# Kernel tuning notes

Hardware: AMD Instinct MI355X
Metric: run time of the kernel (lower is better)

The kernel has to match this reference:

```python
import jax, jax.numpy as jnp
import numpy as np

B, C, D, L, H, K, S, OUT = 8, 2048, 128, 3, 4, 200, 64, 24
d = D // H  # d_head = 32


def _ln(x, g, b):
    m = x.mean(-1, keepdims=True)
    v = ((x - m) ** 2).mean(-1, keepdims=True)
    return (x - m) / jnp.sqrt(v + 1e-5) * g + b


def _gelu(x):
    return jax.nn.gelu(x, approximate=False)  # torch default exact GELU


def setup_inputs() -> dict:
    key = jax.random.key(0)
    ks = iter(jax.random.split(key, 32))
    def nrm(shape, std=0.02):
        return jax.random.normal(next(ks), shape, jnp.float32) * std
    return {
        "x": jax.random.uniform(next(ks), (B, C), jnp.float32) * 5.0,
        "role_emb": nrm((C, D)),
        "filler_w": nrm((D,), 0.1),
        "qW": nrm((L, D, D), 0.05), "qb": jnp.zeros((L, D)),
        "kW": nrm((L, D, D), 0.05), "kb": jnp.zeros((L, D)),
        "vW": nrm((L, D, D), 0.05), "vb": jnp.zeros((L, D)),
        "oW": nrm((L, D, D), 0.05), "ob": jnp.zeros((L, D)),
        "relW1": nrm((L, 3 * d, d), 0.05), "relb1": jnp.zeros((L, d)),
        "relW2": nrm((L, d), 0.05), "relb2": jnp.zeros((L,)),
        "ln1_g": jnp.ones((L, D)), "ln1_b": jnp.zeros((L, D)),
        "ln2_g": jnp.ones((L, D)), "ln2_b": jnp.zeros((L, D)),
        "ffnW1": nrm((L, D, 4 * D), 0.05), "ffnb1": jnp.zeros((L, 4 * D)),
        "ffnW2": nrm((L, 4 * D, D), 0.05), "ffnb2": jnp.zeros((L, D)),
        "slots": nrm((S, D)),
        "memln_g": jnp.ones((D,)), "memln_b": jnp.zeros((D,)),
        "task_q": nrm((D,)),
        "headW": nrm((D, OUT), 0.05), "headb": jnp.zeros((OUT,)),
        "top_k": K,
    }


def _forward(x, role_emb, filler_w, qW, qb, kW, kb, vW, vb, oW, ob,
             relW1, relb1, relW2, relb2, ln1_g, ln1_b, ln2_g, ln2_b,
             ffnW1, ffnb1, ffnW2, ffnb2, slots, memln_g, memln_b,
             task_q, headW, headb, top_k):
    Bx = x.shape[0]
    x_log = jnp.log1p(jnp.maximum(x, 0.0))
    vals, idx = jax.lax.top_k(x_log, top_k)            # [B,K] top intensities
    roles = role_emb[idx]                              # [B,K,D]
    fillers = _gelu(vals[..., None] * filler_w)        # Linear(1,D,bias=False)+GELU
    b = roles * fillers                                # hadamard binding [B,K,D]
    sc_d = jnp.float32(d) ** 0.5
    for l in range(qW.shape[0]):
        q = (b @ qW[l] + qb[l]).reshape(Bx, -1, H, d).transpose(0, 2, 1, 3)
        k = (b @ kW[l] + kb[l]).reshape(Bx, -1, H, d).transpose(0, 2, 1, 3)
        v = (b @ vW[l] + vb[l]).reshape(Bx, -1, H, d).transpose(0, 2, 1, 3)
        # MLP_rel([q_i || k_j || q_i*k_j]) decomposed over the 3d input blocks
        W1q, W1k, W1i = relW1[l][:d], relW1[l][d:2 * d], relW1[l][2 * d:]
        qt = jnp.einsum('bhie,ef->bhif', q, W1q)       # [B,H,K,d]
        kt = jnp.einsum('bhje,ef->bhjf', k, W1k)       # [B,H,K,d]
        itm = jnp.einsum('bhie,bhje,ef->bhijf', q, k, W1i)  # pairwise [B,H,K,K,d]
        hrel = _gelu(qt[:, :, :, None, :] + kt[:, :, None, :, :] + itm + relb1[l])
        scores = (jnp.einsum('bhijf,f->bhij', hrel, relW2[l]) + relb2[l]) / sc_d
        attn = jax.nn.softmax(scores, axis=-1)
        o = jnp.einsum('bhij,bhjd->bhid', attn, v)
        o = o.transpose(0, 2, 1, 3).reshape(Bx, -1, D) @ oW[l] + ob[l]
        b = _ln(b + o, ln1_g[l], ln1_b[l])
        f = _gelu(b @ ffnW1[l] + ffnb1[l]) @ ffnW2[l] + ffnb2[l]
        b = _ln(b + f, ln2_g[l], ln2_b[l])
    sc_D = jnp.float32(D) ** 0.5
    ra = jax.nn.softmax(jnp.einsum('bcd,d->bc', b, task_q) / sc_D, axis=-1)
    h = jnp.einsum('bc,bcd->bd', ra, b)                # task-query readout
    ma = jax.nn.softmax(jnp.einsum('sd,bcd->bsc', slots, b) / sc_D, axis=-1)
    mem = _ln(jnp.einsum('bsc,bcd->bsd', ma, b).mean(axis=1), memln_g, memln_b)
    return (h + mem) @ headW + headb                   # [B,OUT]


def reference(x, role_emb, filler_w, qW, qb, kW, kb, vW, vb, oW, ob,
              relW1, relb1, relW2, relb2, ln1_g, ln1_b, ln2_g, ln2_b,
              ffnW1, ffnb1, ffnW2, ffnb2, slots, memln_g, memln_b,
              task_q, headW, headb, top_k):
    return _forward(x, role_emb, filler_w, qW, qb, kW, kb, vW, vb, oW, ob,
                    relW1, relb1, relW2, relb2, ln1_g, ln1_b, ln2_g, ln2_b,
                    ffnW1, ffnb1, ffnW2, ffnb2, slots, memln_g, memln_b,
                    task_q, headW, headb, top_k)
```

## Files before the change

kernel.cpp:

```cpp
#include <hip/hip_runtime.h>
#include <math.h>

#define BQ 8
#define CC 2048
#define DDIM 128
#define LLAY 3
#define HH 4
#define KK 200
#define SSLOT 64
#define OUTN 24
#define DH 32

typedef __bf16 bf16_t;
typedef __bf16 bf16x8 __attribute__((ext_vector_type(8)));
typedef float f32x4 __attribute__((ext_vector_type(4)));

__device__ __forceinline__ float fastrcp(float x) {
#if __has_builtin(__builtin_amdgcn_rcpf)
  return __builtin_amdgcn_rcpf(x);
#else
  return 1.0f / x;
#endif
}
__device__ __forceinline__ float fastexp2(float x) {
#if __has_builtin(__builtin_amdgcn_exp2f)
  return __builtin_amdgcn_exp2f(x);
#else
  return exp2f(x);
#endif
}
__device__ __forceinline__ float fgelu2(float x) {
  float s = x * x;
  float inner = fmaf(0.044715f * s, x, x);
  float e = fastexp2(inner * 2.302118610509359f);
  float r = fastrcp(1.f + e);
  return fmaf(-x, r, x);
}
__device__ __forceinline__ float egelu(float x) {
  return 0.5f * x * (1.f + erff(x * 0.7071067811865476f));
}

__global__ __launch_bounds__(256) void prep_kernel(
    const float* __restrict__ qW, const float* __restrict__ kW,
    const float* __restrict__ vW, const float* __restrict__ oW,
    const float* __restrict__ fW1, const float* __restrict__ fW2,
    bf16_t* __restrict__ wtb,
    const float* __restrict__ x, const float* __restrict__ role_emb,
    const float* __restrict__ fw, float* __restrict__ btok,
    bf16_t* __restrict__ btokbf) {
  __shared__ float Ts[64][65];
  __shared__ float svals[KK];
  __shared__ int sidx[KK];
  __shared__ int red[4];
  __shared__ int cnt;
  const int blk = blockIdx.x, tid = threadIdx.x;
  if (blk < 144) {
    const int t = blk;
    const float* src; bf16_t* dst; int N, K, k0, n0;
    if (t < 48) {
      int which = t / 12, rem = t % 12;
      int l = rem >> 2, tt = rem & 3;
      N = 128; K = 128; k0 = (tt >> 1) * 64; n0 = (tt & 1) * 64;
      src = (which == 0 ? qW : which == 1 ? kW : which == 2 ? vW : oW) + l * 16384;
      dst = wtb + which * 49152 + l * 16384;
    } else if (t < 96) {
      int t2 = t - 48, l = t2 >> 4, tt = t2 & 15;
      N = 512; K = 128; k0 = (tt >> 3) * 64; n0 = (tt & 7) * 64;
      src = fW1 + l * 65536;
      dst = wtb + 196608 + l * 65536;
    } else {
      int t3 = t - 96, l = t3 >> 4, tt = t3 & 15;
      N = 128; K = 512; k0 = (tt >> 1) * 64; n0 = (tt & 1) * 64;
      src = fW2 + l * 65536;
      dst = wtb + 393216 + l * 65536;
    }
#pragma unroll
    for (int i = 0; i < 16; ++i) {
      int u = tid + i * 256;
      int r = u >> 6, c = u & 63;
      Ts[r][c] = src[(size_t)(k0 + r) * N + n0 + c];
    }
    __syncthreads();
#pragma unroll
    for (int i = 0; i < 16; ++i) {
      int u = tid + i * 256;
      int rn = u >> 6, ck = u & 63;
      dst[(size_t)(n0 + rn) * K + k0 + ck] = (bf16_t)Ts[ck][rn];
    }
    return;
  }
  const int b = blk - 144;
  float xv[8]; unsigned xb[8];
#pragma unroll
  for (int t = 0; t < 8; t++) {
    float v = x[b * CC + t * 256 + tid];
    xv[t] = v;
    xb[t] = __float_as_uint(v);
  }
  unsigned lo = 0u, hi = 0x7f800000u;
  while (lo < hi) {
    unsigned mid = (lo + hi) >> 1;
    int c = 0;
#pragma unroll
    for (int t = 0; t < 8; t++) c += (xb[t] > mid) ? 1 : 0;
#pragma unroll
    for (int m = 1; m <= 32; m <<= 1) c += __shfl_xor(c, m);
    if ((tid & 63) == 0) red[tid >> 6] = c;
    __syncthreads();
    int ct = red[0] + red[1] + red[2] + red[3];
    __syncthreads();
    if (ct >= KK) lo = mid + 1; else hi = mid;
  }
  const unsigned thr = lo;
  if (tid == 0) cnt = 0;
  __syncthreads();
#pragma unroll
  for (int t = 0; t < 8; t++) {
    if (xb[t] > thr) {
      int p = atomicAdd(&cnt, 1);
      svals[p] = log1pf(xv[t]);
      sidx[p] = t * 256 + tid;
    }
  }
  __syncthreads();
#pragma unroll
  for (int t = 0; t < 8; t++) {
    if (xb[t] == thr) {
      int p = atomicAdd(&cnt, 1);
      if (p < KK) {
        svals[p] = log1pf(xv[t]);
        sidx[p] = t * 256 + tid;
      }
    }
  }
  __syncthreads();
  for (int u = tid; u < KK * DDIM; u += 256) {
    int dd = u & 127, t = u >> 7;
    float v = svals[t];
    float fill = egelu(v * fw[dd]);
    float val = role_emb[(size_t)sidx[t] * DDIM + dd] * fill;
    btok[(size_t)b * KK * DDIM + u] = val;
    btokbf[(size_t)b * KK * DDIM + u] = (bf16_t)val;
  }
}

__global__ __launch_bounds__(256) void qkv_mfma(const bf16_t* __restrict__ A,
    const bf16_t* __restrict__ qWt, const float* __restrict__ qb,
    const bf16_t* __restrict__ kWt, const float* __restrict__ kb,
    const bf16_t* __restrict__ vWt, const float* __restrict__ vb,
    bf16_t* __restrict__ qo, bf16_t* __restrict__ ko, bf16_t* __restrict__ vo) {
  __shared__ __align__(16) bf16_t Alds[32 * 16 * 8];
  __shared__ __align__(16) bf16_t Blds[128 * 16 * 8];
  const int tid = threadIdx.x, m0 = blockIdx.x * 32, z = blockIdx.y;
  const bf16_t* Wt; const float* bias; bf16_t* C;
  if (z == 0) { Wt = qWt; bias = qb; C = qo; }
  else if (z == 1) { Wt = kWt; bias = kb; C = ko; }
  else { Wt = vWt; bias = vb; C = vo; }
#pragma unroll
  for (int it = 0; it < 2; ++it) {
    int u = tid + it * 256;
    int row = u >> 4, kc = u & 15;
    uint4 d = *(const uint4*)(A + (size_t)(m0 + row) * 128 + kc * 8);
    *(uint4*)&Alds[(row * 16 + (kc ^ (row & 7))) * 8] = d;
  }
#pragma unroll
  for (int it = 0; it < 8; ++it) {
    int u = tid + it * 256;
    int col = u >> 4, kcb = u & 15;
    uint4 d = *(const uint4*)(Wt + (size_t)col * 128 + kcb * 8);
    *(uint4*)&Blds[(col * 16 + (kcb ^ (col & 7))) * 8] = d;
  }
  __syncthreads();
  const int w = tid >> 6, lane = tid & 63, fcol = lane & 15, g = lane >> 4;
  const int wr = w & 1, wn = w >> 1;
  f32x4 acc[4];
#pragma unroll
  for (int ni = 0; ni < 4; ++ni) acc[ni] = (f32x4){0.f, 0.f, 0.f, 0.f};
#pragma unroll
  for (int ks = 0; ks < 4; ++ks) {
    const int arow = 16 * wr + fcol;
    bf16x8 a = *(const bf16x8*)&Alds[(arow * 16 + ((ks * 4 + g) ^ (arow & 7))) * 8];
#pragma unroll
    for (int ni = 0; ni < 4; ++ni) {
      const int bcol = wn * 64 + ni * 16 + fcol;
      bf16x8 b = *(const bf16x8*)&Blds[(bcol * 16 + ((ks * 4 + g) ^ (bcol & 7))) * 8];
      acc[ni] = __builtin_amdgcn_mfma_f32_16x16x32_bf16(a, b, acc[ni], 0, 0, 0);
    }
  }
#pragma unroll
  for (int ni = 0; ni < 4; ++ni) {
    const int col = wn * 64 + ni * 16 + fcol;
    const float bv = bias[col];
#pragma unroll
    for (int r = 0; r < 4; ++r) {
      const int row = m0 + 16 * wr + 4 * g + r;
      C[(size_t)row * 128 + col] = (bf16_t)(acc[ni][r] + bv);
    }
  }
}

__global__ __launch_bounds__(256, 3) void rel_attn_mfma(
    const bf16_t* __restrict__ qbf, const bf16_t* __restrict__ kbf,
    const bf16_t* __restrict__ vbf,
    const float* __restrict__ W1g, const float* __restrict__ b1g,
    const float* __restrict__ w2p, bf16_t* __restrict__ o) {
  __shared__ __align__(16) bf16_t ksh[208 * 32];
  __shared__ __align__(16) bf16_t vtsh[32 * 224];
  __shared__ __align__(16) bf16_t psh[8 * 224];
  __shared__ __align__(16) bf16_t W1ki[32 * 66];
  __shared__ __align__(16) bf16_t qsh[8 * 32];
  __shared__ __align__(16) bf16_t qtshb[8 * 32];
  const int tid = threadIdx.x;
  const int bh = blockIdx.y, bb = bh >> 2, h = bh & 3;
  const int i0 = blockIdx.x * 8;
  const bf16_t* kgb = kbf + (size_t)(bb * KK) * DDIM + h * DH;
  const bf16_t* vgb = vbf + (size_t)(bb * KK) * DDIM + h * DH;
  const bf16_t* qgb = qbf + (size_t)(bb * KK) * DDIM + h * DH;
#pragma unroll
  for (int it = 0; it < 4; ++it) {
    int u = tid + it * 256;
    if (u < 832) {
      int j = u >> 2, bi = u & 3;
      uint4 d = {0u, 0u, 0u, 0u};
      if (j < KK) d = *(const uint4*)(kgb + (size_t)j * DDIM + bi * 8);
      *(uint4*)&ksh[j * 32 + (bi ^ ((j >> 1) & 3)) * 8] = d;
    }
  }
#pragma unroll
  for (int it = 0; it < 13; ++it) {
    int u = tid + it * 256;
    int jp = u >> 5, f = u & 31;
    int j0 = jp * 2;
    bf16_t a0 = (j0 < KK) ? vgb[(size_t)j0 * DDIM + f] : (bf16_t)0.f;
    bf16_t a1 = (j0 + 1 < KK) ? vgb[(size_t)(j0 + 1) * DDIM + f] : (bf16_t)0.f;
    union { bf16_t h2[2]; unsigned uu; } pk;
    pk.h2[0] = a0; pk.h2[1] = a1;
    *(unsigned*)&vtsh[f * 224 + j0] = pk.uu;
  }
  {
    int f = tid >> 3, cp = tid & 7;
    *(unsigned*)&vtsh[f * 224 + 208 + cp * 2] = 0u;
  }
  if (tid < 64) {
    int r = tid >> 3, cp = tid & 7;
    *(unsigned*)&psh[r * 224 + 208 + cp * 2] = 0u;
  }
#pragma unroll
  for (int it = 0; it < 8; ++it) {
    int u = tid + it * 256;
    int sel = u & 1, f = (u >> 1) & 31, e = u >> 6;
    W1ki[e * 66 + f * 2 + sel] = (bf16_t)W1g[(32 + sel * 32 + e) * 32 + f];
  }
  if (tid < 128) {
    int il = tid >> 4, ep = tid & 15;
    *(unsigned*)&qsh[il * 32 + ep * 2] =
        *(const unsigned*)(qgb + (size_t)(i0 + il) * DDIM + ep * 2);
  }
  __syncthreads();
  {
    int il = tid >> 5, f = tid & 31;
    float a = b1g[f];
#pragma unroll
    for (int e = 0; e < 32; ++e)
      a = fmaf((float)qsh[il * 32 + e], W1g[e * 32 + f], a);
    qtshb[il * 32 + f] = (bf16_t)a;
  }
  __syncthreads();
  const int w = tid >> 6, lane = tid & 63;
  const int fcol = lane & 15, g = lane >> 4;
  const float w2c = 0.17677669529663687f * 1.4426950408889634f;
  float4 w2a = *(const float4*)(w2p + 4 * g);
  float4 w2b = *(const float4*)(w2p + 16 + 4 * g);
  w2a.x *= w2c; w2a.y *= w2c; w2a.z *= w2c; w2a.w *= w2c;
  w2b.x *= w2c; w2b.y *= w2c; w2b.z *= w2c; w2b.w *= w2c;
#pragma unroll 1
  for (int c = 0; c < 2; ++c) {
    const int il = w * 2 + c;
    bf16x8 qv8 = *(const bf16x8*)&qsh[il * 32 + g * 8];
    bf16x8 bw0, bw1;
#pragma unroll
    for (int e8 = 0; e8 < 8; ++e8) {
      int e = g * 8 + e8;
      float qe = (float)qv8[e8];
      union { unsigned u; bf16_t h[2]; } k0_, k1_;
      k0_.u = *(const unsigned*)&W1ki[e * 66 + fcol * 2];
      k1_.u = *(const unsigned*)&W1ki[e * 66 + (fcol + 16) * 2];
      bw0[e8] = (bf16_t)fmaf(qe, (float)k0_.h[1], (float)k0_.h[0]);
      bw1[e8] = (bf16_t)fmaf(qe, (float)k1_.h[1], (float)k1_.h[0]);
    }
    const bf16_t* qtp = &qtshb[il * 32];
    const f32x4 cin0 = {(float)qtp[4 * g + 0], (float)qtp[4 * g + 1],
                        (float)qtp[4 * g + 2], (float)qtp[4 * g + 3]};
    const f32x4 cin1 = {(float)qtp[16 + 4 * g + 0], (float)qtp[16 + 4 * g + 1],
                        (float)qtp[16 + 4 * g + 2], (float)qtp[16 + 4 * g + 3]};
    float s[13];
#pragma unroll
    for (int jt = 0; jt < 13; ++jt) {
      int j = jt * 16 + fcol;
      bf16x8 af = *(const bf16x8*)&ksh[j * 32 + (g ^ ((j >> 1) & 3)) * 8];
      f32x4 acc0 = __builtin_amdgcn_mfma_f32_16x16x32_bf16(bw0, af, cin0, 0, 0, 0);
      f32x4 acc1 = __builtin_amdgcn_mfma_f32_16x16x32_bf16(bw1, af, cin1, 0, 0, 0);
      float t0 = fgelu2(acc0[0]) * w2a.x;
      t0 = fmaf(fgelu2(acc0[1]), w2a.y, t0);
      float t1 = fgelu2(acc0[2]) * w2a.z;
      t1 = fmaf(fgelu2(acc0[3]), w2a.w, t1);
      float t2 = fgelu2(acc1[0]) * w2b.x;
      t2 = fmaf(fgelu2(acc1[1]), w2b.y, t2);
      float t3 = fgelu2(acc1[2]) * w2b.z;
      t3 = fmaf(fgelu2(acc1[3]), w2b.w, t3);
      float t = (t0 + t1) + (t2 + t3);
      t += __shfl_xor(t, 16);
      t += __shfl_xor(t, 32);
      s[jt] = t;
    }
    if (fcol >= 8) s[12] = -1e30f;
    float m = s[0];
#pragma unroll
    for (int jt = 1; jt < 13; ++jt) m = fmaxf(m, s[jt]);
    m = fmaxf(m, __shfl_xor(m, 1));
    m = fmaxf(m, __shfl_xor(m, 2));
    m = fmaxf(m, __shfl_xor(m, 4));
    m = fmaxf(m, __shfl_xor(m, 8));
    float l = 0.f;
#pragma unroll
    for (int jt = 0; jt < 13; ++jt) {
      float p = fastexp2(s[jt] - m);
      s[jt] = p;
      l += p;
    }
    l += __shfl_xor(l, 1);
    l += __shfl_xor(l, 2);
    l += __shfl_xor(l, 4);
    l += __shfl_xor(l, 8);
    const float inv = fastrcp(l);
    if (g == 0) {
#pragma unroll
      for (int jt = 0; jt < 13; ++jt)
        psh[il * 224 + jt * 16 + fcol] = (bf16_t)(s[jt] * inv);
    }
  }
  __syncthreads();
  if (w < 2) {
    f32x4 acc = {0.f, 0.f, 0.f, 0.f};
#pragma unroll
    for (int ks = 0; ks < 7; ++ks) {
      bf16x8 ap;
      if (fcol < 8) ap = *(const bf16x8*)&psh[fcol * 224 + ks * 32 + g * 8];
      else { bf16x8 z = {}; ap = z; }
      bf16x8 bv = *(const bf16x8*)&vtsh[(w * 16 + fcol) * 224 + ks * 32 + g * 8];
      acc = __builtin_amdgcn_mfma_f32_16x16x32_bf16(ap, bv, acc, 0, 0, 0);
    }
    if (g < 2) {
#pragma unroll
      for (int r = 0; r < 4; ++r) {
        int i = i0 + g * 4 + r;
        o[(size_t)(bb * KK + i) * DDIM + h * DH + w * 16 + fcol] = (bf16_t)acc[r];
      }
    }
  }
}

__global__ __launch_bounds__(512) void tail_fused(const bf16_t* __restrict__ obufbf,
    const bf16_t* __restrict__ oWt, const float* __restrict__ ob,
    const float* __restrict__ ln1g, const float* __restrict__ ln1b,
    const bf16_t* __restrict__ W1t, const float* __restrict__ b1,
    const bf16_t* __restrict__ W2t, const float* __restrict__ b2,
    const float* __restrict__ ln2g, const float* __restrict__ ln2b,
    float* __restrict__ btok, bf16_t* __restrict__ btokbf,
    const bf16_t* __restrict__ nqWt, const float* __restrict__ nqb,
    const bf16_t* __restrict__ nkWt, const float* __restrict__ nkb,
    const bf16_t* __restrict__ nvWt, const float* __restrict__ nvb,
    bf16_t* __restrict__ nqo, bf16_t* __restrict__ nko, bf16_t* __restrict__ nvo) {
  __shared__ __align__(16) bf16_t Alds[64 * 16 * 8];
  __shared__ __align__(16) bf16_t Blds[128 * 16 * 8];
  __shared__ __align__(16) bf16_t Hlds[64 * 512];
  __shared__ float lnredS[64][2], lnredQ[64][2];
  const int tid = threadIdx.x, m0 = blockIdx.x * 64;
  const int w = tid >> 6, lane = tid & 63, fcol = lane & 15, g = lane >> 4;
  const int wrow = w & 3, whalf = w >> 2;
#pragma unroll
  for (int it = 0; it < 2; ++it) {
    int u = tid + it * 512;
    int row = u >> 4, kc = u & 15;
    uint4 d = *(const uint4*)(obufbf + (size_t)(m0 + row) * 128 + kc * 8);
    *(uint4*)&Alds[(row * 16 + (kc ^ (row & 7))) * 8] = d;
  }
#pragma unroll
  for (int it = 0; it < 4; ++it) {
    int u = tid + it * 512;
    int col = u >> 4, kcb = u & 15;
    uint4 d = *(const uint4*)(oWt + (size_t)col * 128 + kcb * 8);
    *(uint4*)&Blds[(col * 16 + (kcb ^ (col & 7))) * 8] = d;
  }
  __syncthreads();
  f32x4 acc[4];
#pragma unroll
  for (int ni = 0; ni < 4; ++ni) acc[ni] = (f32x4){0.f, 0.f, 0.f, 0.f};
  const int arow = 16 * wrow + fcol;
#pragma unroll
  for (int ks = 0; ks < 4; ++ks) {
    bf16x8 a = *(const bf16x8*)&Alds[(arow * 16 + ((ks * 4 + g) ^ (arow & 7))) * 8];
#pragma unroll
    for (int ni = 0; ni < 4; ++ni) {
      const int bcol = whalf * 64 + ni * 16 + fcol;
      bf16x8 b = *(const bf16x8*)&Blds[(bcol * 16 + ((ks * 4 + g) ^ (bcol & 7))) * 8];
      acc[ni] = __builtin_amdgcn_mfma_f32_16x16x32_bf16(a, b, acc[ni], 0, 0, 0);
    }
  }
  float lnr[4][4];
  {
    float s_[4] = {0.f, 0.f, 0.f, 0.f}, q_[4] = {0.f, 0.f, 0.f, 0.f};
#pragma unroll
    for (int ni = 0; ni < 4; ++ni) {
      const int col = whalf * 64 + ni * 16 + fcol;
      const float bv = ob[col];
#pragma unroll
      for (int r = 0; r < 4; ++r) {
        const int row = m0 + 16 * wrow + 4 * g + r;
        float val = acc[ni][r] + bv + btok[(size_t)row * 128 + col];
        lnr[ni][r] = val;
        s_[r] += val; q_[r] += val * val;
      }
    }
#pragma unroll
    for (int m = 1; m <= 8; m <<= 1)
#pragma unroll
      for (int r = 0; r < 4; ++r) {
        s_[r] += __shfl_xor(s_[r], m); q_[r] += __shfl_xor(q_[r], m);
      }
    if (fcol == 0) {
#pragma unroll
      for (int r = 0; r < 4; ++r) {
        lnredS[16 * wrow + 4 * g + r][whalf] = s_[r];
        lnredQ[16 * wrow + 4 * g + r][whalf] = q_[r];
      }
    }
    __syncthreads();
    float mean[4], rs[4];
#pragma unroll
    for (int r = 0; r < 4; ++r) {
      const int rl = 16 * wrow + 4 * g + r;
      float S = lnredS[rl][0] + lnredS[rl][1];
      float Q = lnredQ[rl][0] + lnredQ[rl][1];
      mean[r] = S * (1.f / 128.f);
      rs[r] = rsqrtf(Q * (1.f / 128.f) - mean[r] * mean[r] + 1e-5f);
    }
#pragma unroll
    for (int ni = 0; ni < 4; ++ni) {
      const int col = whalf * 64 + ni * 16 + fcol;
      const float gv = ln1g[col], bv2 = ln1b[col];
#pragma unroll
      for (int r = 0; r < 4; ++r) {
        float v2 = (lnr[ni][r] - mean[r]) * rs[r] * gv + bv2;
        lnr[ni][r] = v2;
        const int rowL = 16 * wrow + 4 * g + r;
        Alds[(rowL * 16 + ((col >> 3) ^ (rowL & 7))) * 8 + (col & 7)] = (bf16_t)v2;
      }
    }
  }
  __syncthreads();
  for (int nc = 0; nc < 4; ++nc) {
#pragma unroll
    for (int it = 0; it < 4; ++it) {
      int u = tid + it * 512;
      int col = u >> 4, kcb = u & 15;
      uint4 d = *(const uint4*)(W1t + (size_t)(nc * 128 + col) * 128 + kcb * 8);
      *(uint4*)&Blds[(col * 16 + (kcb ^ (col & 7))) * 8] = d;
    }
    __syncthreads();
    f32x4 a1[4];
#pragma unroll
    for (int ni = 0; ni < 4; ++ni) a1[ni] = (f32x4){0.f, 0.f, 0.f, 0.f};
#pragma unroll
    for (int ks = 0; ks < 4; ++ks) {
      bf16x8 a = *(const bf16x8*)&Alds[(arow * 16 + ((ks * 4 + g) ^ (arow & 7))) * 8];
#pragma unroll
      for (int ni = 0; ni < 4; ++ni) {
        const int bcol = whalf * 64 + ni * 16 + fcol;
        bf16x8 b = *(const bf16x8*)&Blds[(bcol * 16 + ((ks * 4 + g) ^ (bcol & 7))) * 8];
        a1[ni] = __builtin_amdgcn_mfma_f32_16x16x32_bf16(a, b, a1[ni], 0, 0, 0);
      }
    }
#pragma unroll
    for (int ni = 0; ni < 4; ++ni) {
      const int c = nc * 128 + whalf * 64 + ni * 16 + fcol;
      const float bv = b1[c];
      const int kb = c >> 3, within = c & 7;
#pragma unroll
      for (int r = 0; r < 4; ++r) {
        const int row = 16 * wrow + 4 * g + r;
        const int kbs = kb ^ (row & 7);
        Hlds[row * 512 + kbs * 8 + within] = (bf16_t)egelu(a1[ni][r] + bv);
      }
    }
    __syncthreads();
  }
  f32x4 acc2[4];
#pragma unroll
  for (int ni = 0; ni < 4; ++ni) acc2[ni] = (f32x4){0.f, 0.f, 0.f, 0.f};
  for (int kc = 0; kc < 4; ++kc) {
#pragma unroll
    for (int it = 0; it < 4; ++it) {
      int u = tid + it * 512;
      int col = u >> 4, kcb = u & 15;
      uint4 d = *(const uint4*)(W2t + (size_t)col * 512 + kc * 128 + kcb * 8);
      *(uint4*)&Blds[(col * 16 + (kcb ^ (col & 7))) * 8] = d;
    }
    __syncthreads();
#pragma unroll
    for (int ks = 0; ks < 4; ++ks) {
      const int kb = kc * 16 + ks * 4 + g;
      const int kbs = kb ^ (arow & 7);
      bf16x8 a = *(const bf16x8*)&Hlds[arow * 512 + kbs * 8];
#pragma unroll
      for (int ni = 0; ni < 4; ++ni) {
        const int bcol = whalf * 64 + ni * 16 + fcol;
        bf16x8 b = *(const bf16x8*)&Blds[(bcol * 16 + ((ks * 4 + g) ^ (bcol & 7))) * 8];
        acc2[ni] = __builtin_amdgcn_mfma_f32_16x16x32_bf16(a, b, acc2[ni], 0, 0, 0);
      }
    }
    __syncthreads();
  }
  {
    float s_[4] = {0.f, 0.f, 0.f, 0.f}, q_[4] = {0.f, 0.f, 0.f, 0.f};
#pragma unroll
    for (int ni = 0; ni < 4; ++ni) {
      const int col = whalf * 64 + ni * 16 + fcol;
      const float bv = b2[col];
#pragma unroll
      for (int r = 0; r < 4; ++r) {
        float val = acc2[ni][r] + bv + lnr[ni][r];
        lnr[ni][r] = val;
        s_[r] += val; q_[r] += val * val;
      }
    }
#pragma unroll
    for (int m = 1; m <= 8; m <<= 1)
#pragma unroll
      for (int r = 0; r < 4; ++r) {
        s_[r] += __shfl_xor(s_[r], m); q_[r] += __shfl_xor(q_[r], m);
      }
    if (fcol == 0) {
#pragma unroll
      for (int r = 0; r < 4; ++r) {
        lnredS[16 * wrow + 4 * g + r][whalf] = s_[r];
        lnredQ[16 * wrow + 4 * g + r][whalf] = q_[r];
      }
    }
    __syncthreads();
    float mean[4], rs[4];
#pragma unroll
    for (int r = 0; r < 4; ++r) {
      const int rl = 16 * wrow + 4 * g + r;
      float S = lnredS[rl][0] + lnredS[rl][1];
      float Q = lnredQ[rl][0] + lnredQ[rl][1];
      mean[r] = S * (1.f / 128.f);
      rs[r] = rsqrtf(Q * (1.f / 128.f) - mean[r] * mean[r] + 1e-5f);
    }
#pragma unroll
    for (int ni = 0; ni < 4; ++ni) {
      const int col = whalf * 64 + ni * 16 + fcol;
      const float gv = ln2g[col], bv2 = ln2b[col];
#pragma unroll
      for (int r = 0; r < 4; ++r) {
        const int row = m0 + 16 * wrow + 4 * g + r;
        float oval = (lnr[ni][r] - mean[r]) * rs[r] * gv + bv2;
        btok[(size_t)row * 128 + col] = oval;
        btokbf[(size_t)row * 128 + col] = (bf16_t)oval;
        if (nqWt) {
          const int rowL = 16 * wrow + 4 * g + r;
          Alds[(rowL * 16 + ((col >> 3) ^ (rowL & 7))) * 8 + (col & 7)] = (bf16_t)oval;
        }
      }
    }
  }
  if (nqWt) {
    __syncthreads();
    const bf16_t* Ws[3] = {nqWt, nkWt, nvWt};
    const float* bs[3] = {nqb, nkb, nvb};
    bf16_t* Cs[3] = {nqo, nko, nvo};
    for (int zz = 0; zz < 3; ++zz) {
      const bf16_t* Wt = Ws[zz];
#pragma unroll
      for (int it = 0; it < 4; ++it) {
        int u = tid + it * 512;
        int col = u >> 4, kcb = u & 15;
        uint4 d = *(const uint4*)(Wt + (size_t)col * 128 + kcb * 8);
        *(uint4*)&Blds[(col * 16 + (kcb ^ (col & 7))) * 8] = d;
      }
      __syncthreads();
      f32x4 aq[4];
#pragma unroll
      for (int ni = 0; ni < 4; ++ni) aq[ni] = (f32x4){0.f, 0.f, 0.f, 0.f};
#pragma unroll
      for (int ks = 0; ks < 4; ++ks) {
        bf16x8 a = *(const bf16x8*)&Alds[(arow * 16 + ((ks * 4 + g) ^ (arow & 7))) * 8];
#pragma unroll
        for (int ni = 0; ni < 4; ++ni) {
          const int bcol = whalf * 64 + ni * 16 + fcol;
          bf16x8 b = *(const bf16x8*)&Blds[(bcol * 16 + ((ks * 4 + g) ^ (bcol & 7))) * 8];
          aq[ni] = __builtin_amdgcn_mfma_f32_16x16x32_bf16(a, b, aq[ni], 0, 0, 0);
        }
      }
      const float* bias = bs[zz];
      bf16_t* C = Cs[zz];
#pragma unroll
      for (int ni = 0; ni < 4; ++ni) {
        const int col = whalf * 64 + ni * 16 + fcol;
        const float bv = bias[col];
#pragma unroll
        for (int r = 0; r < 4; ++r) {
          const int row = m0 + 16 * wrow + 4 * g + r;
          C[(size_t)row * 128 + col] = (bf16_t)(aq[ni][r] + bv);
        }
      }
      __syncthreads();
    }
  }
}

__global__ __launch_bounds__(256) void readout_fused(const float* __restrict__ B,
    const bf16_t* __restrict__ Bbf, const float* __restrict__ slots,
    const float* __restrict__ task_q, const float* __restrict__ memg,
    const float* __restrict__ membt, const float* __restrict__ headW,
    const float* __restrict__ headb, float* __restrict__ out) {
  __shared__ __align__(16) bf16_t Ssh[64 * 16 * 8];
  __shared__ __align__(16) bf16_t Bsh[208 * 128];
  __shared__ float wcsh[4][208];
  __shared__ __align__(16) float tq[128];
  __shared__ float ras[KK];
  __shared__ float wc[208];
  __shared__ float red1[4], red2[4];
  __shared__ float hv2[256], mv2[256];
  __shared__ float hv[128], mv[128], rv[128];
  __shared__ float stats[2];
  const int b = blockIdx.x, tid = threadIdx.x;
  const int w = tid >> 6, lane = tid & 63, fcol = lane & 15, g = lane >> 4;
#pragma unroll
  for (int it = 0; it < 4; ++it) {
    int u = tid + it * 256;
    int row = u >> 4, kb = u & 15;
    const float* sp = slots + (size_t)row * 128 + kb * 8;
    bf16_t tmp[8];
#pragma unroll
    for (int e = 0; e < 8; ++e) tmp[e] = (bf16_t)sp[e];
    *(uint4*)&Ssh[(row * 16 + (kb ^ (row & 7))) * 8] = *(uint4*)tmp;
  }
#pragma unroll
  for (int it = 0; it < 13; ++it) {
    int u = tid + it * 256;
    int c = u >> 4, kb = u & 15;
    uint4 d = {0u, 0u, 0u, 0u};
    if (c < KK) d = *(const uint4*)(Bbf + (size_t)(b * KK + c) * 128 + kb * 8);
    *(uint4*)&Bsh[(c * 16 + (kb ^ (c & 7))) * 8] = d;
  }
  if (tid < 128) tq[tid] = task_q[tid];
  __syncthreads();
  {
    bf16x8 afr[4];
#pragma unroll
    for (int ks = 0; ks < 4; ++ks) {
      const int arow = 16 * w + fcol;
      afr[ks] = *(const bf16x8*)&Ssh[(arow * 16 + ((ks * 4 + g) ^ (arow & 7))) * 8];
    }
    f32x4 acc[13];
#pragma unroll
    for (int ct = 0; ct < 13; ++ct) {
      acc[ct] = (f32x4){0.f, 0.f, 0.f, 0.f};
#pragma unroll
      for (int ks = 0; ks < 4; ++ks) {
        const int bcol = ct * 16 + fcol;
        bf16x8 bb = *(const bf16x8*)&Bsh[(bcol * 16 + ((ks * 4 + g) ^ (bcol & 7))) * 8];
        acc[ct] = __builtin_amdgcn_mfma_f32_16x16x32_bf16(afr[ks], bb, acc[ct], 0, 0, 0);
      }
    }
    if (fcol >= 8) { acc[12][0] = -1e30f; acc[12][1] = -1e30f; acc[12][2] = -1e30f; acc[12][3] = -1e30f; }
    const float s2 = 0.08838834764831845f * 1.4426950408889634f;
    float wcp[13];
#pragma unroll
    for (int ct = 0; ct < 13; ++ct) wcp[ct] = 0.f;
#pragma unroll
    for (int r = 0; r < 4; ++r) {
      float m = acc[0][r];
#pragma unroll
      for (int ct = 1; ct < 13; ++ct) m = fmaxf(m, acc[ct][r]);
      m = fmaxf(m, __shfl_xor(m, 1));
      m = fmaxf(m, __shfl_xor(m, 2));
      m = fmaxf(m, __shfl_xor(m, 4));
      m = fmaxf(m, __shfl_xor(m, 8));
      float l = 0.f;
      float p[13];
#pragma unroll
      for (int ct = 0; ct < 13; ++ct) {
        p[ct] = fastexp2((acc[ct][r] - m) * s2);
        l += p[ct];
      }
      l += __shfl_xor(l, 1);
      l += __shfl_xor(l, 2);
      l += __shfl_xor(l, 4);
      l += __shfl_xor(l, 8);
      const float inv = fastrcp(l);
#pragma unroll
      for (int ct = 0; ct < 13; ++ct) wcp[ct] = fmaf(p[ct], inv, wcp[ct]);
    }
#pragma unroll
    for (int ct = 0; ct < 13; ++ct) {
      wcp[ct] += __shfl_xor(wcp[ct], 16);
      wcp[ct] += __shfl_xor(wcp[ct], 32);
      if (g == 0) wcsh[w][ct * 16 + fcol] = wcp[ct];
    }
  }
  float sc = -1e30f;
  if (tid < KK) {
    const float* br = B + (size_t)(b * KK + tid) * DDIM;
    float a = 0.f;
#pragma unroll
    for (int d4 = 0; d4 < 32; d4++) {
      float4 bb = *(const float4*)(br + d4 * 4);
      float4 ss = *(const float4*)(tq + d4 * 4);
      a += bb.x * ss.x + bb.y * ss.y + bb.z * ss.z + bb.w * ss.w;
    }
    sc = a * 0.08838834764831845f;
  }
  float mx = sc;
#pragma unroll
  for (int m = 1; m <= 32; m <<= 1) mx = fmaxf(mx, __shfl_xor(mx, m));
  if ((tid & 63) == 0) red1[tid >> 6] = mx;
  __syncthreads();
  mx = fmaxf(fmaxf(red1[0], red1[1]), fmaxf(red1[2], red1[3]));
  float p = (tid < KK) ? __expf(sc - mx) : 0.f;
  float sm = p;
#pragma unroll
  for (int m = 1; m <= 32; m <<= 1) sm += __shfl_xor(sm, m);
  if ((tid & 63) == 0) red2[tid >> 6] = sm;
  __syncthreads();
  sm = red2[0] + red2[1] + red2[2] + red2[3];
  if (tid < KK) ras[tid] = p / sm;
  if (tid < 208)
    wc[tid] = (wcsh[0][tid] + wcsh[1][tid] + wcsh[2][tid] + wcsh[3][tid]) * (1.f / 64.f);
  __syncthreads();
  {
    const int d = tid & 127, half = tid >> 7;
    float hd = 0.f, md = 0.f;
    const float* Bb = B + ((size_t)b * KK + half * 100) * DDIM + d;
    const float* rp = ras + half * 100;
    const float* wp = wc + half * 100;
#pragma unroll 2
    for (int c = 0; c < 100; ++c) {
      float bv = Bb[(size_t)c * DDIM];
      hd = fmaf(rp[c], bv, hd);
      md = fmaf(wp[c], bv, md);
    }
    hv2[tid] = hd; mv2[tid] = md;
  }
  __syncthreads();
  if (tid < 128) {
    hv[tid] = hv2[tid] + hv2[tid + 128];
    mv[tid] = mv2[tid] + mv2[tid + 128];
  }
  __syncthreads();
  if (tid < 64) {
    float x0 = mv[tid], x1 = mv[tid + 64];
    float s = x0 + x1, qq = x0 * x0 + x1 * x1;
#pragma unroll
    for (int m = 1; m <= 32; m <<= 1) { s += __shfl_xor(s, m); qq += __shfl_xor(qq, m); }
    if (tid == 0) { stats[0] = s; stats[1] = qq; }
  }
  __syncthreads();
  float mean = stats[0] * (1.f / 128.f);
  float var = stats[1] * (1.f / 128.f) - mean * mean;
  float rs = rsqrtf(var + 1e-5f);
  if (tid < 128) rv[tid] = hv[tid] + (mv[tid] - mean) * rs * memg[tid] + membt[tid];
  __syncthreads();
  if (tid < OUTN) {
    float a = headb[tid];
    for (int dd = 0; dd < 128; dd++) a = fmaf(rv[dd], headW[dd * OUTN + tid], a);
    out[b * OUTN + tid] = a;
  }
}

extern "C" void kernel_launch(void* const* d_in, const int* in_sizes, int n_in,
                              void* d_out, int out_size, void* d_ws, size_t ws_size,
                              hipStream_t stream) {
  (void)in_sizes; (void)n_in; (void)out_size; (void)ws_size;
  const float* x        = (const float*)d_in[0];
  const float* role_emb = (const float*)d_in[1];
  const float* filler_w = (const float*)d_in[2];
  const float* qW = (const float*)d_in[3];
  const float* qb = (const float*)d_in[4];
  const float* kW = (const float*)d_in[5];
  const float* kb = (const float*)d_in[6];
  const float* vW = (const float*)d_in[7];
  const float* vb = (const float*)d_in[8];
  const float* oW = (const float*)d_in[9];
  const float* ob = (const float*)d_in[10];
  const float* relW1 = (const float*)d_in[11];
  const float* relb1 = (const float*)d_in[12];
  const float* relW2 = (const float*)d_in[13];
  const float* relb2 = (const float*)d_in[14];
  const float* ln1g = (const float*)d_in[15];
  const float* ln1b = (const float*)d_in[16];
  const float* ln2g = (const float*)d_in[17];
  const float* ln2b = (const float*)d_in[18];
  const float* fW1 = (const float*)d_in[19];
  const float* fb1 = (const float*)d_in[20];
  const float* fW2 = (const float*)d_in[21];
  const float* fb2 = (const float*)d_in[22];
  const float* slots = (const float*)d_in[23];
  const float* memg = (const float*)d_in[24];
  const float* memb = (const float*)d_in[25];
  const float* taskq = (const float*)d_in[26];
  const float* headW = (const float*)d_in[27];
  const float* headb = (const float*)d_in[28];
  float* out = (float*)d_out;
  (void)relb2;

  float* fws  = (float*)d_ws;
  float*  btok   = fws;
  bf16_t* btokbf = (bf16_t*)(fws + 204800);
  bf16_t* qbf    = (bf16_t*)(fws + 307200);
  bf16_t* kbf    = (bf16_t*)(fws + 409600);
  bf16_t* vbf    = (bf16_t*)(fws + 512000);
  bf16_t* obufbf = (bf16_t*)(fws + 614400);
  bf16_t* wtb    = (bf16_t*)(fws + 716800);
  bf16_t* qWt = wtb, *kWt = wtb + 49152, *vWt = wtb + 98304, *oWt = wtb + 147456;
  bf16_t* fW1t = wtb + 196608, *fW2t = wtb + 393216;

  prep_kernel<<<152, 256, 0, stream>>>(qW, kW, vW, oW, fW1, fW2, wtb,
      x, role_emb, filler_w, btok, btokbf);
  qkv_mfma<<<dim3(50, 3), 256, 0, stream>>>(btokbf,
      qWt, qb, kWt, kb, vWt, vb, qbf, kbf, vbf);
  for (int l = 0; l < LLAY; l++) {
    rel_attn_mfma<<<dim3(25, 32), 256, 0, stream>>>(qbf, kbf, vbf,
        relW1 + l * 3072, relb1 + l * 32, relW2 + l * 32, obufbf);
    const bool nx = (l + 1 < LLAY);
    tail_fused<<<25, 512, 0, stream>>>(obufbf, oWt + l * 16384, ob + l * 128,
        ln1g + l * 128, ln1b + l * 128, fW1t + l * 65536, fb1 + l * 512,
        fW2t + l * 65536, fb2 + l * 128, ln2g + l * 128, ln2b + l * 128,
        btok, btokbf,
        nx ? qWt + (l + 1) * 16384 : (const bf16_t*)nullptr,
        nx ? qb + (l + 1) * 128 : (const float*)nullptr,
        nx ? kWt + (l + 1) * 16384 : (const bf16_t*)nullptr,
        nx ? kb + (l + 1) * 128 : (const float*)nullptr,
        nx ? vWt + (l + 1) * 16384 : (const bf16_t*)nullptr,
        nx ? vb + (l + 1) * 128 : (const float*)nullptr,
        qbf, kbf, vbf);
  }
  readout_fused<<<8, 256, 0, stream>>>(btok, btokbf, slots, taskq,
      memg, memb, headW, headb, out);
}
```

Measured before the change: 238.6 us.

## Widen rel_attn blocks to one row per wave and halve tail_fused row tiles

rel_attn_mfma now launches 512 threads, so each of its 8 waves handles a single query row instead of looping over two, and the cooperative loads are re-strided to match. tail_fused processes 32 rows per block instead of 64, launching 50 blocks, with each wave covering a 16x32 output slice and LayerNorm partial sums reduced across four column quarters. The aim is more parallelism on a GPU that was mostly idle with 25 blocks, plus lower per-wave latency in attention. In exchange, per-block weight loads are duplicated across twice as many tail blocks, and the larger attention blocks may lower occupancy.

After: 218.2 us. -8.5%, faster.

```diff
diff --git a/kernel.cpp b/kernel.cpp
--- a/kernel.cpp
+++ b/kernel.cpp
@@ -199,7 +199,7 @@
   }
 }
 
-__global__ __launch_bounds__(256, 3) void rel_attn_mfma(
+__global__ __launch_bounds__(512, 4) void rel_attn_mfma(
     const bf16_t* __restrict__ qbf, const bf16_t* __restrict__ kbf,
     const bf16_t* __restrict__ vbf,
     const float* __restrict__ W1g, const float* __restrict__ b1g,
@@ -217,8 +217,8 @@
   const bf16_t* vgb = vbf + (size_t)(bb * KK) * DDIM + h * DH;
   const bf16_t* qgb = qbf + (size_t)(bb * KK) * DDIM + h * DH;
 #pragma unroll
-  for (int it = 0; it < 4; ++it) {
-    int u = tid + it * 256;
+  for (int it = 0; it < 2; ++it) {
+    int u = tid + it * 512;
     if (u < 832) {
       int j = u >> 2, bi = u & 3;
       uint4 d = {0u, 0u, 0u, 0u};
@@ -227,17 +227,19 @@
     }
   }
 #pragma unroll
-  for (int it = 0; it < 13; ++it) {
-    int u = tid + it * 256;
-    int jp = u >> 5, f = u & 31;
-    int j0 = jp * 2;
-    bf16_t a0 = (j0 < KK) ? vgb[(size_t)j0 * DDIM + f] : (bf16_t)0.f;
-    bf16_t a1 = (j0 + 1 < KK) ? vgb[(size_t)(j0 + 1) * DDIM + f] : (bf16_t)0.f;
-    union { bf16_t h2[2]; unsigned uu; } pk;
-    pk.h2[0] = a0; pk.h2[1] = a1;
-    *(unsigned*)&vtsh[f * 224 + j0] = pk.uu;
-  }
-  {
+  for (int it = 0; it < 7; ++it) {
+    int u = tid + it * 512;
+    if (u < 3328) {
+      int jp = u >> 5, f = u & 31;
+      int j0 = jp * 2;
+      bf16_t a0 = (j0 < KK) ? vgb[(size_t)j0 * DDIM + f] : (bf16_t)0.f;
+      bf16_t a1 = (j0 + 1 < KK) ? vgb[(size_t)(j0 + 1) * DDIM + f] : (bf16_t)0.f;
+      union { bf16_t h2[2]; unsigned uu; } pk;
+      pk.h2[0] = a0; pk.h2[1] = a1;
+      *(unsigned*)&vtsh[f * 224 + j0] = pk.uu;
+    }
+  }
+  if (tid < 256) {
     int f = tid >> 3, cp = tid & 7;
     *(unsigned*)&vtsh[f * 224 + 208 + cp * 2] = 0u;
   }
@@ -246,8 +248,8 @@
     *(unsigned*)&psh[r * 224 + 208 + cp * 2] = 0u;
   }
 #pragma unroll
-  for (int it = 0; it < 8; ++it) {
-    int u = tid + it * 256;
+  for (int it = 0; it < 4; ++it) {
+    int u = tid + it * 512;
     int sel = u & 1, f = (u >> 1) & 31, e = u >> 6;
     W1ki[e * 66 + f * 2 + sel] = (bf16_t)W1g[(32 + sel * 32 + e) * 32 + f];
   }
@@ -257,7 +259,7 @@
         *(const unsigned*)(qgb + (size_t)(i0 + il) * DDIM + ep * 2);
   }
   __syncthreads();
-  {
+  if (tid < 256) {
     int il = tid >> 5, f = tid & 31;
     float a = b1g[f];
 #pragma unroll
@@ -273,9 +275,8 @@
   float4 w2b = *(const float4*)(w2p + 16 + 4 * g);
   w2a.x *= w2c; w2a.y *= w2c; w2a.z *= w2c; w2a.w *= w2c;
   w2b.x *= w2c; w2b.y *= w2c; w2b.z *= w2c; w2b.w *= w2c;
-#pragma unroll 1
-  for (int c = 0; c < 2; ++c) {
-    const int il = w * 2 + c;
+  {
+    const int il = w;
     bf16x8 qv8 = *(const bf16x8*)&qsh[il * 32 + g * 8];
     bf16x8 bw0, bw1;
 #pragma unroll
@@ -371,16 +372,16 @@
     const bf16_t* __restrict__ nkWt, const float* __restrict__ nkb,
     const bf16_t* __restrict__ nvWt, const float* __restrict__ nvb,
     bf16_t* __restrict__ nqo, bf16_t* __restrict__ nko, bf16_t* __restrict__ nvo) {
-  __shared__ __align__(16) bf16_t Alds[64 * 16 * 8];
+  __shared__ __align__(16) bf16_t Alds[32 * 16 * 8];
   __shared__ __align__(16) bf16_t Blds[128 * 16 * 8];
-  __shared__ __align__(16) bf16_t Hlds[64 * 512];
-  __shared__ float lnredS[64][2], lnredQ[64][2];
-  const int tid = threadIdx.x, m0 = blockIdx.x * 64;
+  __shared__ __align__(16) bf16_t Hlds[32 * 512];
+  __shared__ float lnredS[32][4], lnredQ[32][4];
+  const int tid = threadIdx.x, m0 = blockIdx.x * 32;
   const int w = tid >> 6, lane = tid & 63, fcol = lane & 15, g = lane >> 4;
-  const int wrow = w & 3, whalf = w >> 2;
-#pragma unroll
-  for (int it = 0; it < 2; ++it) {
-    int u = tid + it * 512;
+  const int wrow = w & 1, wq = w >> 1;
+  const int arow = 16 * wrow + fcol;
+  {
+    int u = tid;
     int row = u >> 4, kc = u & 15;
     uint4 d = *(const uint4*)(obufbf + (size_t)(m0 + row) * 128 + kc * 8);
     *(uint4*)&Alds[(row * 16 + (kc ^ (row & 7))) * 8] = d;
@@ -393,26 +394,25 @@
     *(uint4*)&Blds[(col * 16 + (kcb ^ (col & 7))) * 8] = d;
   }
   __syncthreads();
-  f32x4 acc[4];
-#pragma unroll
-  for (int ni = 0; ni < 4; ++ni) acc[ni] = (f32x4){0.f, 0.f, 0.f, 0.f};
-  const int arow = 16 * wrow + fcol;
+  f32x4 acc[2];
+#pragma unroll
+  for (int ni = 0; ni < 2; ++ni) acc[ni] = (f32x4){0.f, 0.f, 0.f, 0.f};
 #pragma unroll
   for (int ks = 0; ks < 4; ++ks) {
     bf16x8 a = *(const bf16x8*)&Alds[(arow * 16 + ((ks * 4 + g) ^ (arow & 7))) * 8];
 #pragma unroll
-    for (int ni = 0; ni < 4; ++ni) {
-      const int bcol = whalf * 64 + ni * 16 + fcol;
+    for (int ni = 0; ni < 2; ++ni) {
+      const int bcol = wq * 32 + ni * 16 + fcol;
       bf16x8 b = *(const bf16x8*)&Blds[(bcol * 16 + ((ks * 4 + g) ^ (bcol & 7))) * 8];
       acc[ni] = __builtin_amdgcn_mfma_f32_16x16x32_bf16(a, b, acc[ni], 0, 0, 0);
     }
   }
-  float lnr[4][4];
+  float lnr[2][4];
   {
     float s_[4] = {0.f, 0.f, 0.f, 0.f}, q_[4] = {0.f, 0.f, 0.f, 0.f};
 #pragma unroll
-    for (int ni = 0; ni < 4; ++ni) {
-      const int col = whalf * 64 + ni * 16 + fcol;
+    for (int ni = 0; ni < 2; ++ni) {
+      const int col = wq * 32 + ni * 16 + fcol;
       const float bv = ob[col];
 #pragma unroll
       for (int r = 0; r < 4; ++r) {
@@ -431,8 +431,8 @@
     if (fcol == 0) {
 #pragma unroll
       for (int r = 0; r < 4; ++r) {
-        lnredS[16 * wrow + 4 * g + r][whalf] = s_[r];
-        lnredQ[16 * wrow + 4 * g + r][whalf] = q_[r];
+        lnredS[16 * wrow + 4 * g + r][wq] = s_[r];
+        lnredQ[16 * wrow + 4 * g + r][wq] = q_[r];
       }
     }
     __syncthreads();
@@ -440,14 +440,14 @@
 #pragma unroll
     for (int r = 0; r < 4; ++r) {
       const int rl = 16 * wrow + 4 * g + r;
-      float S = lnredS[rl][0] + lnredS[rl][1];
-      float Q = lnredQ[rl][0] + lnredQ[rl][1];
+      float S = lnredS[rl][0] + lnredS[rl][1] + lnredS[rl][2] + lnredS[rl][3];
+      float Q = lnredQ[rl][0] + lnredQ[rl][1] + lnredQ[rl][2] + lnredQ[rl][3];
       mean[r] = S * (1.f / 128.f);
       rs[r] = rsqrtf(Q * (1.f / 128.f) - mean[r] * mean[r] + 1e-5f);
     }
 #pragma unroll
-    for (int ni = 0; ni < 4; ++ni) {
-      const int col = whalf * 64 + ni * 16 + fcol;
+    for (int ni = 0; ni < 2; ++ni) {
+      const int col = wq * 32 + ni * 16 + fcol;
       const float gv = ln1g[col], bv2 = ln1b[col];
 #pragma unroll
       for (int r = 0; r < 4; ++r) {
@@ -468,22 +468,22 @@
       *(uint4*)&Blds[(col * 16 + (kcb ^ (col & 7))) * 8] = d;
     }
     __syncthreads();
-    f32x4 a1[4];
-#pragma unroll
-    for (int ni = 0; ni < 4; ++ni) a1[ni] = (f32x4){0.f, 0.f, 0.f, 0.f};
+    f32x4 a1[2];
+#pragma unroll
+    for (int ni = 0; ni < 2; ++ni) a1[ni] = (f32x4){0.f, 0.f, 0.f, 0.f};
 #pragma unroll
     for (int ks = 0; ks < 4; ++ks) {
       bf16x8 a = *(const bf16x8*)&Alds[(arow * 16 + ((ks * 4 + g) ^ (arow & 7))) * 8];
 #pragma unroll
-      for (int ni = 0; ni < 4; ++ni) {
-        const int bcol = whalf * 64 + ni * 16 + fcol;
+      for (int ni = 0; ni < 2; ++ni) {
+        const int bcol = wq * 32 + ni * 16 + fcol;
         bf16x8 b = *(const bf16x8*)&Blds[(bcol * 16 + ((ks * 4 + g) ^ (bcol & 7))) * 8];
         a1[ni] = __builtin_amdgcn_mfma_f32_16x16x32_bf16(a, b, a1[ni], 0, 0, 0);
       }
     }
 #pragma unroll
-    for (int ni = 0; ni < 4; ++ni) {
-      const int c = nc * 128 + whalf * 64 + ni * 16 + fcol;
+    for (int ni = 0; ni < 2; ++ni) {
+      const int c = nc * 128 + wq * 32 + ni * 16 + fcol;
       const float bv = b1[c];
       const int kb = c >> 3, within = c & 7;
 #pragma unroll
@@ -495,9 +495,9 @@
     }
     __syncthreads();
   }
-  f32x4 acc2[4];
-#pragma unroll
-  for (int ni = 0; ni < 4; ++ni) acc2[ni] = (f32x4){0.f, 0.f, 0.f, 0.f};
+  f32x4 acc2[2];
+#pragma unroll
+  for (int ni = 0; ni < 2; ++ni) acc2[ni] = (f32x4){0.f, 0.f, 0.f, 0.f};
   for (int kc = 0; kc < 4; ++kc) {
 #pragma unroll
     for (int it = 0; it < 4; ++it) {
@@ -513,8 +513,8 @@
       const int kbs = kb ^ (arow & 7);
       bf16x8 a = *(const bf16x8*)&Hlds[arow * 512 + kbs * 8];
 #pragma unroll
-      for (int ni = 0; ni < 4; ++ni) {
-        const int bcol = whalf * 64 + ni * 16 + fcol;
+      for (int ni = 0; ni < 2; ++ni) {
+        const int bcol = wq * 32 + ni * 16 + fcol;
         bf16x8 b = *(const bf16x8*)&Blds[(bcol * 16 + ((ks * 4 + g) ^ (bcol & 7))) * 8];
         acc2[ni] = __builtin_amdgcn_mfma_f32_16x16x32_bf16(a, b, acc2[ni], 0, 0, 0);
       }
@@ -524,8 +524,8 @@
   {
     float s_[4] = {0.f, 0.f, 0.f, 0.f}, q_[4] = {0.f, 0.f, 0.f, 0.f};
 #pragma unroll
-    for (int ni = 0; ni < 4; ++ni) {
-      const int col = whalf * 64 + ni * 16 + fcol;
+    for (int ni = 0; ni < 2; ++ni) {
+      const int col = wq * 32 + ni * 16 + fcol;
       const float bv = b2[col];
 #pragma unroll
       for (int r = 0; r < 4; ++r) {
@@ -543,8 +543,8 @@
     if (fcol == 0) {
 #pragma unroll
       for (int r = 0; r < 4; ++r) {
-        lnredS[16 * wrow + 4 * g + r][whalf] = s_[r];
-        lnredQ[16 * wrow + 4 * g + r][whalf] = q_[r];
+        lnredS[16 * wrow + 4 * g + r][wq] = s_[r];
+        lnredQ[16 * wrow + 4 * g + r][wq] = q_[r];
       }
     }
     __syncthreads();
@@ -552,14 +552,14 @@
 #pragma unroll
     for (int r = 0; r < 4; ++r) {
       const int rl = 16 * wrow + 4 * g + r;
-      float S = lnredS[rl][0] + lnredS[rl][1];
-      float Q = lnredQ[rl][0] + lnredQ[rl][1];
+      float S = lnredS[rl][0] + lnredS[rl][1] + lnredS[rl][2] + lnredS[rl][3];
+      float Q = lnredQ[rl][0] + lnredQ[rl][1] + lnredQ[rl][2] + lnredQ[rl][3];
       mean[r] = S * (1.f / 128.f);
       rs[r] = rsqrtf(Q * (1.f / 128.f) - mean[r] * mean[r] + 1e-5f);
     }
 #pragma unroll
-    for (int ni = 0; ni < 4; ++ni) {
-      const int col = whalf * 64 + ni * 16 + fcol;
+    for (int ni = 0; ni < 2; ++ni) {
+      const int col = wq * 32 + ni * 16 + fcol;
       const float gv = ln2g[col], bv2 = ln2b[col];
 #pragma unroll
       for (int r = 0; r < 4; ++r) {
@@ -589,15 +589,15 @@
         *(uint4*)&Blds[(col * 16 + (kcb ^ (col & 7))) * 8] = d;
       }
       __syncthreads();
-      f32x4 aq[4];
-#pragma unroll
-      for (int ni = 0; ni < 4; ++ni) aq[ni] = (f32x4){0.f, 0.f, 0.f, 0.f};
+      f32x4 aq[2];
+#pragma unroll
+      for (int ni = 0; ni < 2; ++ni) aq[ni] = (f32x4){0.f, 0.f, 0.f, 0.f};
 #pragma unroll
       for (int ks = 0; ks < 4; ++ks) {
         bf16x8 a = *(const bf16x8*)&Alds[(arow * 16 + ((ks * 4 + g) ^ (arow & 7))) * 8];
 #pragma unroll
-        for (int ni = 0; ni < 4; ++ni) {
-          const int bcol = whalf * 64 + ni * 16 + fcol;
+        for (int ni = 0; ni < 2; ++ni) {
+          const int bcol = wq * 32 + ni * 16 + fcol;
           bf16x8 b = *(const bf16x8*)&Blds[(bcol * 16 + ((ks * 4 + g) ^ (bcol & 7))) * 8];
           aq[ni] = __builtin_amdgcn_mfma_f32_16x16x32_bf16(a, b, aq[ni], 0, 0, 0);
         }
@@ -605,8 +605,8 @@
       const float* bias = bs[zz];
       bf16_t* C = Cs[zz];
 #pragma unroll
-      for (int ni = 0; ni < 4; ++ni) {
-        const int col = whalf * 64 + ni * 16 + fcol;
+      for (int ni = 0; ni < 2; ++ni) {
+        const int col = wq * 32 + ni * 16 + fcol;
         const float bv = bias[col];
 #pragma unroll
         for (int r = 0; r < 4; ++r) {
@@ -831,10 +831,10 @@
   qkv_mfma<<<dim3(50, 3), 256, 0, stream>>>(btokbf,
       qWt, qb, kWt, kb, vWt, vb, qbf, kbf, vbf);
   for (int l = 0; l < LLAY; l++) {
-    rel_attn_mfma<<<dim3(25, 32), 256, 0, stream>>>(qbf, kbf, vbf,
+    rel_attn_mfma<<<dim3(25, 32), 512, 0, stream>>>(qbf, kbf, vbf,
         relW1 + l * 3072, relb1 + l * 32, relW2 + l * 32, obufbf);
     const bool nx = (l + 1 < LLAY);
-    tail_fused<<<25, 512, 0, stream>>>(obufbf, oWt + l * 16384, ob + l * 128,
+    tail_fused<<<50, 512, 0, stream>>>(obufbf, oWt + l * 16384, ob + l * 128,
         ln1g + l * 128, ln1b + l * 128, fW1t + l * 65536, fb1 + l * 512,
         fW2t + l * 65536, fb2 + l * 128, ln2g + l * 128, ln2b + l * 128,
         btok, btokbf,
```
